# Kernel optimization log

Hardware: AMD Instinct MI355X
Metric: run time of the kernel (lower is better)

Reference implementation:

```python
import jax, jax.numpy as jnp
import numpy as np

DEC_H = 1024
ENC_H_TOTAL = 1024  # enc_hid_size * enc_num_dirs


def setup_inputs() -> dict:
    key = jax.random.key(0)
    ks = jax.random.split(key, 10)
    N, L = 64, 1024
    s = 0.02
    return {
        "dec_h_curr": jax.random.normal(ks[0], (N, DEC_H), jnp.float32),
        "enc_hids": jax.random.normal(ks[1], (N, L, ENC_H_TOTAL), jnp.float32),
        # project_dec_hids: Linear(dec_H, dec_H)
        "W_dec": jax.random.normal(ks[2], (DEC_H, DEC_H), jnp.float32) * s,
        "b_dec": jnp.zeros((DEC_H,), jnp.float32),
        # project_enc_hids: Linear(enc_H*nDir, dec_H)
        "W_enc": jax.random.normal(ks[3], (ENC_H_TOTAL, DEC_H), jnp.float32) * s,
        "b_enc": jnp.zeros((DEC_H,), jnp.float32),
        # project_to_one_dim: Linear(dec_H, 1)
        "W_one": jax.random.normal(ks[4], (DEC_H, 1), jnp.float32) * s,
        "b_one": jnp.zeros((1,), jnp.float32),
        # project_att_hids: Linear(enc_H*nDir, dec_H)
        "W_att": jax.random.normal(ks[5], (ENC_H_TOTAL, DEC_H), jnp.float32) * s,
        "b_att": jnp.zeros((DEC_H,), jnp.float32),
    }


def reference(dec_h_curr, enc_hids, W_dec, b_dec, W_enc, b_enc, W_one, b_one, W_att, b_att):
    # additive (Bahdanau) attention branch
    d = dec_h_curr @ W_dec + b_dec                     # N x dec_H
    e = jnp.einsum('nle,ed->nld', enc_hids, W_enc) + b_enc  # N x L x dec_H
    scores = jnp.einsum('nld,do->nl', jnp.tanh(d[:, None, :] + e), W_one) + b_one[0]  # N x L
    alpha = jax.nn.softmax(scores, axis=-1)            # N x L
    ctx = jnp.einsum('nl,nle->ne', alpha, enc_hids)    # N x enc_H_total
    h_att_curr = ctx @ W_att + b_att                   # N x dec_H
    return h_att_curr, alpha
```

## Files before the change

### kernel.cpp

```cpp
#include <hip/hip_runtime.h>
#include <cstdio>
#include <cstdint>


typedef __bf16 bf16x8 __attribute__((ext_vector_type(8)));
typedef float f32x4 __attribute__((ext_vector_type(4)));
typedef unsigned short us8 __attribute__((ext_vector_type(8)));

static __device__ __forceinline__ unsigned short f2b(float f) {
  union { float f; unsigned u; } v; v.f = f;
  unsigned r = (v.u + 0x7fffu + ((v.u >> 16) & 1u)) >> 16;
  return (unsigned short)r;
}
static __device__ __forceinline__ float b2f(unsigned short u) {
  union { unsigned u; float f; } v; v.u = ((unsigned)u) << 16;
  return v.f;
}
static __device__ __forceinline__ void gl_lds16(const void* g, void* l) {
  __builtin_amdgcn_global_load_lds(
      (const __attribute__((address_space(1))) unsigned int*)g,
      (__attribute__((address_space(3))) unsigned int*)l, 16, 0, 0);
}
static __device__ __forceinline__ float fast_tanh(float x) {
  float ax = __builtin_fminf(__builtin_fabsf(x), 18.0f);
  float u = __builtin_amdgcn_exp2f(ax * 2.88539008177792681f);
  float t = (u - 1.0f) * __builtin_amdgcn_rcpf(u + 1.0f);
  return __builtin_copysignf(t, x);
}

__global__ __launch_bounds__(256) void prep_k(
    const float* __restrict__ enc, unsigned short* __restrict__ Ap,
    const float* __restrict__ W_enc, unsigned short* __restrict__ Bp,
    const float* __restrict__ dec_h, const float* __restrict__ W_dec,
    const float* __restrict__ b_dec, const float* __restrict__ b_enc,
    float* __restrict__ addterm) {
  __shared__ __align__(16) unsigned short tile[8192];
  const int bid = blockIdx.x;
  const int t = threadIdx.x;

  if (bid < 128) {
    const int Tn = bid >> 4, kt = bid & 15;
    #pragma unroll
    for (int it = 0; it < 8; ++it) {
      int idx = it * 256 + t;
      int kk = idx >> 5, n4 = idx & 31;
      const float4 v = *(const float4*)(W_enc + (size_t)(kt * 64 + kk) * 1024 + Tn * 128 + n4 * 4);
      int c = kk >> 3, j = kk & 7;
      #pragma unroll
      for (int x = 0; x < 4; ++x) {
        int mm = n4 * 4 + x;
        float fv = (x == 0) ? v.x : (x == 1) ? v.y : (x == 2) ? v.z : v.w;
        tile[(mm * 8 + (c ^ (mm & 7))) * 8 + j] = f2b(fv);
      }
    }
    __syncthreads();
    #pragma unroll
    for (int it = 0; it < 4; ++it) {
      int p = it * 256 + t;
      int c = p >> 7, m = p & 127;
      us8 v = *(const us8*)&tile[(m * 8 + (c ^ (m & 7))) * 8];
      *(us8*)(Bp + ((size_t)bid * 1024 + p) * 8) = v;
    }
  } else if (bid < 384) {
    const int bid2 = bid - 128;
    const int jb = bid2 & 3, n = bid2 >> 2;
    float* xs = (float*)tile;
    for (int i = t; i < 1024; i += 256) xs[i] = dec_h[n * 1024 + i];
    __syncthreads();
    int j = jb * 256 + t;
    float s = 0.f;
    #pragma unroll 8
    for (int k = 0; k < 1024; ++k) s += xs[k] * W_dec[(size_t)k * 1024 + j];
    addterm[n * 1024 + j] = s + b_dec[j] + b_enc[j];
  } else {
    const int ba = bid - 384;
    const int T = ba >> 4, kt = ba & 15;
    #pragma unroll
    for (int it = 0; it < 8; ++it) {
      int idx = it * 256 + t;
      int m = idx >> 4, c4 = idx & 15;
      const float4 v = *(const float4*)(enc + (size_t)(T * 128 + m) * 1024 + kt * 64 + c4 * 4);
      ushort4 o;
      o.x = f2b(v.x); o.y = f2b(v.y); o.z = f2b(v.z); o.w = f2b(v.w);
      int c = c4 >> 1, half = c4 & 1;
      *(ushort4*)&tile[(m * 8 + (c ^ (m & 7))) * 8 + half * 4] = o;
    }
    __syncthreads();
    #pragma unroll
    for (int it = 0; it < 4; ++it) {
      int p = it * 256 + t;
      int c = p >> 7, m = p & 127;
      us8 v = *(const us8*)&tile[(m * 8 + (c ^ (m & 7))) * 8];
      *(us8*)(Ap + ((size_t)ba * 1024 + p) * 8) = v;
    }
  }
}

__global__ __launch_bounds__(256) void score_gemm(
    const unsigned short* __restrict__ Ap, const unsigned short* __restrict__ Bp,
    const float* __restrict__ addterm, const float* __restrict__ Wone,
    float* __restrict__ spart) {
  __shared__ __align__(16) unsigned short lA[8192];
  __shared__ __align__(16) unsigned short lB[8192];
  const int tid = threadIdx.x;
  const int lane = tid & 63, wave = tid >> 6;
  const int wm = wave >> 1, wn = wave & 1;
  const int q = lane >> 4, r = lane & 15;
  const int flat = blockIdx.x;
  const int nb = (flat >> 3) & 7;
  const int mb = ((flat >> 6) << 3) + (flat & 7);
  const size_t tileM = (size_t)mb * 128;
  const int tileN = nb * 128;

  f32x4 acc[4][4];
  #pragma unroll
  for (int i = 0; i < 4; ++i)
    #pragma unroll
    for (int j = 0; j < 4; ++j) acc[i][j] = (f32x4){0.f, 0.f, 0.f, 0.f};

  const unsigned short* gA[2][2];
  const unsigned short* gB[2][2];
  unsigned short* dA[2][2];
  unsigned short* dB[2][2];
  #pragma unroll
  for (int cc = 0; cc < 2; ++cc) {
    int c = wave * 2 + cc;
    #pragma unroll
    for (int i = 0; i < 2; ++i) {
      gA[cc][i] = Ap + ((((size_t)mb * 16) * 8 + c) * 128 + i * 64 + lane) * 8;
      gB[cc][i] = Bp + ((((size_t)nb * 16) * 8 + c) * 128 + i * 64 + lane) * 8;
      dA[cc][i] = &lA[(c * 128 + i * 64) * 8];
      dB[cc][i] = &lB[(c * 128 + i * 64) * 8];
    }
  }

  for (int kt = 0; kt < 16; ++kt) {
    __syncthreads();
    const size_t ko = (size_t)kt * 8192;
    gl_lds16(gA[0][0] + ko, dA[0][0]);
    gl_lds16(gA[0][1] + ko, dA[0][1]);
    gl_lds16(gA[1][0] + ko, dA[1][0]);
    gl_lds16(gA[1][1] + ko, dA[1][1]);
    gl_lds16(gB[0][0] + ko, dB[0][0]);
    gl_lds16(gB[0][1] + ko, dB[0][1]);
    gl_lds16(gB[1][0] + ko, dB[1][0]);
    gl_lds16(gB[1][1] + ko, dB[1][1]);
    __syncthreads();
    #pragma unroll
    for (int s = 0; s < 2; ++s) {
      bf16x8 af[4], bg[4];
      #pragma unroll
      for (int mi = 0; mi < 4; ++mi)
        af[mi] = *(const bf16x8*)&lA[((s * 4 + q) * 128 + wm * 64 + mi * 16 + r) * 8];
      #pragma unroll
      for (int ni = 0; ni < 4; ++ni)
        bg[ni] = *(const bf16x8*)&lB[((s * 4 + q) * 128 + wn * 64 + ni * 16 + r) * 8];
      #pragma unroll
      for (int mi = 0; mi < 4; ++mi)
        #pragma unroll
        for (int ni = 0; ni < 4; ++ni)
          acc[mi][ni] = __builtin_amdgcn_mfma_f32_16x16x32_bf16(af[mi], bg[ni], acc[mi][ni], 0, 0, 0);
    }
  }

  const int nrow = (int)(tileM >> 10);
  float addv[4], wv[4];
  #pragma unroll
  for (int ni = 0; ni < 4; ++ni) {
    int col = tileN + wn * 64 + ni * 16 + r;
    addv[ni] = addterm[nrow * 1024 + col];
    wv[ni] = Wone[col];
  }
  #pragma unroll
  for (int mi = 0; mi < 4; ++mi) {
    #pragma unroll
    for (int rr = 0; rr < 4; ++rr) {
      float s = 0.f;
      #pragma unroll
      for (int ni = 0; ni < 4; ++ni)
        s += fast_tanh(acc[mi][ni][rr] + addv[ni]) * wv[ni];
      s += __shfl_xor(s, 1);
      s += __shfl_xor(s, 2);
      s += __shfl_xor(s, 4);
      s += __shfl_xor(s, 8);
      if (r == 0) {
        size_t row = tileM + wm * 64 + mi * 16 + q * 4 + rr;
        spart[row * 16 + nb * 2 + wn] = s;
      }
    }
  }
}

__global__ __launch_bounds__(256) void ctx_fused(
    const float* __restrict__ spart, float* __restrict__ alpha,
    const unsigned short* __restrict__ Ap, float* __restrict__ ctx) {
  const int kt = blockIdx.x, n = blockIdx.y, t = threadIdx.x;
  __shared__ float red[8];
  __shared__ float al[1024];

  float sv[4];
  #pragma unroll
  for (int i = 0; i < 4; ++i) {
    int l = i * 256 + t;
    const float4* p = (const float4*)(spart + ((size_t)n * 1024 + l) * 16);
    float4 v0 = p[0], v1 = p[1], v2 = p[2], v3 = p[3];
    sv[i] = (v0.x + v0.y + v0.z + v0.w) + (v1.x + v1.y + v1.z + v1.w) +
            (v2.x + v2.y + v2.z + v2.w) + (v3.x + v3.y + v3.z + v3.w);
  }
  float m = fmaxf(fmaxf(sv[0], sv[1]), fmaxf(sv[2], sv[3]));
  for (int o = 32; o > 0; o >>= 1) m = fmaxf(m, __shfl_xor(m, o));
  if ((t & 63) == 0) red[t >> 6] = m;
  __syncthreads();
  float gm = fmaxf(fmaxf(red[0], red[1]), fmaxf(red[2], red[3]));
  float e[4], s = 0.f;
  #pragma unroll
  for (int i = 0; i < 4; ++i) { e[i] = expf(sv[i] - gm); s += e[i]; }
  for (int o = 32; o > 0; o >>= 1) s += __shfl_xor(s, o);
  if ((t & 63) == 0) red[4 + (t >> 6)] = s;
  __syncthreads();
  float inv = 1.0f / (red[4] + red[5] + red[6] + red[7]);
  #pragma unroll
  for (int i = 0; i < 4; ++i) {
    float a = e[i] * inv;
    al[i * 256 + t] = a;
    if (kt == 0) alpha[(size_t)n * 1024 + i * 256 + t] = a;
  }
  __syncthreads();

  const int c = t >> 5, ls = t & 31;
  float acc[8] = {0.f, 0.f, 0.f, 0.f, 0.f, 0.f, 0.f, 0.f};
  #pragma unroll 4
  for (int lb = 0; lb < 32; ++lb) {
    int l = lb * 32 + ls;
    int M = n * 1024 + l;
    int T = M >> 7, mm = M & 127;
    us8 v = *(const us8*)(Ap + ((((size_t)T * 16 + kt) * 8 + c) * 128 + mm) * 8);
    float w = al[l];
    #pragma unroll
    for (int j = 0; j < 8; ++j) acc[j] += w * b2f(v[j]);
  }
  #pragma unroll
  for (int off = 1; off <= 16; off <<= 1)
    #pragma unroll
    for (int j = 0; j < 8; ++j) acc[j] += __shfl_xor(acc[j], off);
  if (ls == 0) {
    #pragma unroll
    for (int j = 0; j < 8; ++j) ctx[(size_t)n * 1024 + kt * 64 + c * 8 + j] = acc[j];
  }
}

__global__ void hatt_k(const float* __restrict__ ctx, const float* __restrict__ W_att,
                       const float* __restrict__ b_att, float* __restrict__ out) {
  __shared__ float cs[1024];
  int n = blockIdx.y;
  int j = blockIdx.x * 256 + threadIdx.x;
  for (int i = threadIdx.x; i < 1024; i += 256) cs[i] = ctx[(size_t)n * 1024 + i];
  __syncthreads();
  float s = 0.f;
  #pragma unroll 8
  for (int k = 0; k < 1024; ++k) s += cs[k] * W_att[(size_t)k * 1024 + j];
  out[n * 1024 + j] = s + b_att[j];
}

extern "C" void kernel_launch(void* const* d_in, const int* in_sizes, int n_in,
                              void* d_out, int out_size, void* d_ws, size_t ws_size,
                              hipStream_t stream) {
  const float* dec_h = (const float*)d_in[0];
  const float* enc   = (const float*)d_in[1];
  const float* W_dec = (const float*)d_in[2];
  const float* b_dec = (const float*)d_in[3];
  const float* W_enc = (const float*)d_in[4];
  const float* b_enc = (const float*)d_in[5];
  const float* W_one = (const float*)d_in[6];
  const float* W_att = (const float*)d_in[8];
  const float* b_att = (const float*)d_in[9];
  float* out = (float*)d_out;

  char* ws = (char*)d_ws;
  const size_t OFF_A   = 0;
  const size_t OFF_B   = 134217728;
  const size_t OFF_ADD = OFF_B + 2097152;
  const size_t OFF_SP  = OFF_ADD + 262144;
  const size_t OFF_CTX = OFF_SP + 4194304;
  const size_t NEED    = OFF_CTX + 262144;
  if (ws_size < NEED) {
    fprintf(stderr, "kernel_launch: ws too small (%zu < %zu)\n", ws_size, NEED);
    return;
  }
  unsigned short* Ap = (unsigned short*)(ws + OFF_A);
  unsigned short* Bp = (unsigned short*)(ws + OFF_B);
  float* addterm = (float*)(ws + OFF_ADD);
  float* spart   = (float*)(ws + OFF_SP);
  float* ctx     = (float*)(ws + OFF_CTX);
  float* alpha   = out + 65536;

  prep_k<<<8576, 256, 0, stream>>>(enc, Ap, W_enc, Bp, dec_h, W_dec, b_dec, b_enc, addterm);
  score_gemm<<<4096, 256, 0, stream>>>(Ap, Bp, addterm, W_one, spart);
  ctx_fused<<<dim3(16, 64), 256, 0, stream>>>(spart, alpha, Ap, ctx);
  hatt_k<<<dim3(4, 64), 256, 0, stream>>>(ctx, W_att, b_att, out);
}
```

Baseline: 692.7 us.

## Restructure score GEMM into 256x256 double-buffered pipelined tiles; split-K hatt

The score GEMM moves from 128x128 tiles with 4 waves to 256x256 tiles with 8 waves. It adds LDS double buffering, interleaved async global-to-LDS loads placed between MFMA groups, explicit vmcnt waits and s_setprio around MFMA bursts, plus a remapped block order. The intent is to hide load latency and raise arithmetic intensity on the dominant GEMM, at the cost of larger LDS use and hand-tuned waitcnt correctness risk. The hatt kernel is also split along K across 4 waves with a shared-memory reduction, giving 4x more blocks for parallelism.

```diff
diff --git a/kernel.cpp b/kernel.cpp
--- a/kernel.cpp
+++ b/kernel.cpp
@@ -96,83 +96,123 @@
   }
 }
 
-__global__ __launch_bounds__(256) void score_gemm(
+__global__ __launch_bounds__(512, 2) void score_gemm(
     const unsigned short* __restrict__ Ap, const unsigned short* __restrict__ Bp,
     const float* __restrict__ addterm, const float* __restrict__ Wone,
     float* __restrict__ spart) {
-  __shared__ __align__(16) unsigned short lA[8192];
-  __shared__ __align__(16) unsigned short lB[8192];
+  __shared__ __align__(16) unsigned short lA[32768];
+  __shared__ __align__(16) unsigned short lB[32768];
   const int tid = threadIdx.x;
   const int lane = tid & 63, wave = tid >> 6;
-  const int wm = wave >> 1, wn = wave & 1;
+  const int wm = wave >> 2, wn = wave & 3;
   const int q = lane >> 4, r = lane & 15;
+
   const int flat = blockIdx.x;
-  const int nb = (flat >> 3) & 7;
-  const int mb = ((flat >> 6) << 3) + (flat & 7);
-  const size_t tileM = (size_t)mb * 128;
-  const int tileN = nb * 128;
-
-  f32x4 acc[4][4];
-  #pragma unroll
-  for (int i = 0; i < 4; ++i)
+  const int tl = (flat & 7) * 128 + (flat >> 3);
+  const int nb = tl & 3, mb = tl >> 2;
+
+  f32x4 acc[8][4];
+  #pragma unroll
+  for (int i = 0; i < 8; ++i)
     #pragma unroll
     for (int j = 0; j < 4; ++j) acc[i][j] = (f32x4){0.f, 0.f, 0.f, 0.f};
 
-  const unsigned short* gA[2][2];
-  const unsigned short* gB[2][2];
-  unsigned short* dA[2][2];
-  unsigned short* dB[2][2];
-  #pragma unroll
-  for (int cc = 0; cc < 2; ++cc) {
-    int c = wave * 2 + cc;
-    #pragma unroll
-    for (int i = 0; i < 2; ++i) {
-      gA[cc][i] = Ap + ((((size_t)mb * 16) * 8 + c) * 128 + i * 64 + lane) * 8;
-      gB[cc][i] = Bp + ((((size_t)nb * 16) * 8 + c) * 128 + i * 64 + lane) * 8;
-      dA[cc][i] = &lA[(c * 128 + i * 64) * 8];
-      dB[cc][i] = &lB[(c * 128 + i * 64) * 8];
-    }
-  }
-
-  for (int kt = 0; kt < 16; ++kt) {
-    __syncthreads();
-    const size_t ko = (size_t)kt * 8192;
-    gl_lds16(gA[0][0] + ko, dA[0][0]);
-    gl_lds16(gA[0][1] + ko, dA[0][1]);
-    gl_lds16(gA[1][0] + ko, dA[1][0]);
-    gl_lds16(gA[1][1] + ko, dA[1][1]);
-    gl_lds16(gB[0][0] + ko, dB[0][0]);
-    gl_lds16(gB[0][1] + ko, dB[0][1]);
-    gl_lds16(gB[1][0] + ko, dB[1][0]);
-    gl_lds16(gB[1][1] + ko, dB[1][1]);
-    __syncthreads();
-    #pragma unroll
-    for (int s = 0; s < 2; ++s) {
-      bf16x8 af[4], bg[4];
-      #pragma unroll
-      for (int mi = 0; mi < 4; ++mi)
-        af[mi] = *(const bf16x8*)&lA[((s * 4 + q) * 128 + wm * 64 + mi * 16 + r) * 8];
-      #pragma unroll
-      for (int ni = 0; ni < 4; ++ni)
-        bg[ni] = *(const bf16x8*)&lB[((s * 4 + q) * 128 + wn * 64 + ni * 16 + r) * 8];
-      #pragma unroll
-      for (int mi = 0; mi < 4; ++mi)
-        #pragma unroll
-        for (int ni = 0; ni < 4; ++ni)
-          acc[mi][ni] = __builtin_amdgcn_mfma_f32_16x16x32_bf16(af[mi], bg[ni], acc[mi][ni], 0, 0, 0);
-    }
-  }
-
-  const int nrow = (int)(tileM >> 10);
+  const unsigned short* gA0 = Ap + (((size_t)(2 * mb + 0) * 16) * 1024 + tid) * 8;
+  const unsigned short* gA1 = Ap + (((size_t)(2 * mb + 1) * 16) * 1024 + tid) * 8;
+  const unsigned short* gB0 = Bp + (((size_t)(2 * nb + 0) * 16) * 1024 + tid) * 8;
+  const unsigned short* gB1 = Bp + (((size_t)(2 * nb + 1) * 16) * 1024 + tid) * 8;
+
+  const unsigned short* rdA = &lA[(wm * 1024 + q * 128 + r) * 8];
+  const unsigned short* rdB = &lB[((wn >> 1) * 1024 + q * 128 + (wn & 1) * 64 + r) * 8];
+
+  bf16x8 af[4], bg[4];
+
+#define SA(h, t, s) gl_lds16((h ? gA1 : gA0) + ((size_t)(t) * 1024 + (s) * 512) * 8, \
+                             &lA[((((t) & 1) * 2048 + (h) * 1024 + (s) * 512 + wave * 64) * 8)])
+#define SB(h, t, s) gl_lds16((h ? gB1 : gB0) + ((size_t)(t) * 1024 + (s) * 512) * 8, \
+                             &lB[((((t) & 1) * 2048 + (h) * 1024 + (s) * 512 + wave * 64) * 8)])
+#define RD_BG(b, s) { \
+  bg[0] = *(const bf16x8*)&rdB[((b) * 2048 + (s) * 512 +  0) * 8]; \
+  bg[1] = *(const bf16x8*)&rdB[((b) * 2048 + (s) * 512 + 16) * 8]; \
+  bg[2] = *(const bf16x8*)&rdB[((b) * 2048 + (s) * 512 + 32) * 8]; \
+  bg[3] = *(const bf16x8*)&rdB[((b) * 2048 + (s) * 512 + 48) * 8]; }
+#define RD_AF(b, s, mh) { \
+  af[0] = *(const bf16x8*)&rdA[((b) * 2048 + (s) * 512 + (mh) * 64 +  0) * 8]; \
+  af[1] = *(const bf16x8*)&rdA[((b) * 2048 + (s) * 512 + (mh) * 64 + 16) * 8]; \
+  af[2] = *(const bf16x8*)&rdA[((b) * 2048 + (s) * 512 + (mh) * 64 + 32) * 8]; \
+  af[3] = *(const bf16x8*)&rdA[((b) * 2048 + (s) * 512 + (mh) * 64 + 48) * 8]; }
+#define MMA_CORE(mh) \
+  __builtin_amdgcn_s_barrier(); \
+  asm volatile("s_waitcnt lgkmcnt(0)" ::: "memory"); \
+  __builtin_amdgcn_s_setprio(1); \
+  acc[(mh)*4+0][0] = __builtin_amdgcn_mfma_f32_16x16x32_bf16(af[0], bg[0], acc[(mh)*4+0][0], 0, 0, 0); \
+  acc[(mh)*4+0][1] = __builtin_amdgcn_mfma_f32_16x16x32_bf16(af[0], bg[1], acc[(mh)*4+0][1], 0, 0, 0); \
+  acc[(mh)*4+0][2] = __builtin_amdgcn_mfma_f32_16x16x32_bf16(af[0], bg[2], acc[(mh)*4+0][2], 0, 0, 0); \
+  acc[(mh)*4+0][3] = __builtin_amdgcn_mfma_f32_16x16x32_bf16(af[0], bg[3], acc[(mh)*4+0][3], 0, 0, 0); \
+  acc[(mh)*4+1][0] = __builtin_amdgcn_mfma_f32_16x16x32_bf16(af[1], bg[0], acc[(mh)*4+1][0], 0, 0, 0); \
+  acc[(mh)*4+1][1] = __builtin_amdgcn_mfma_f32_16x16x32_bf16(af[1], bg[1], acc[(mh)*4+1][1], 0, 0, 0); \
+  acc[(mh)*4+1][2] = __builtin_amdgcn_mfma_f32_16x16x32_bf16(af[1], bg[2], acc[(mh)*4+1][2], 0, 0, 0); \
+  acc[(mh)*4+1][3] = __builtin_amdgcn_mfma_f32_16x16x32_bf16(af[1], bg[3], acc[(mh)*4+1][3], 0, 0, 0); \
+  acc[(mh)*4+2][0] = __builtin_amdgcn_mfma_f32_16x16x32_bf16(af[2], bg[0], acc[(mh)*4+2][0], 0, 0, 0); \
+  acc[(mh)*4+2][1] = __builtin_amdgcn_mfma_f32_16x16x32_bf16(af[2], bg[1], acc[(mh)*4+2][1], 0, 0, 0); \
+  acc[(mh)*4+2][2] = __builtin_amdgcn_mfma_f32_16x16x32_bf16(af[2], bg[2], acc[(mh)*4+2][2], 0, 0, 0); \
+  acc[(mh)*4+2][3] = __builtin_amdgcn_mfma_f32_16x16x32_bf16(af[2], bg[3], acc[(mh)*4+2][3], 0, 0, 0); \
+  acc[(mh)*4+3][0] = __builtin_amdgcn_mfma_f32_16x16x32_bf16(af[3], bg[0], acc[(mh)*4+3][0], 0, 0, 0); \
+  acc[(mh)*4+3][1] = __builtin_amdgcn_mfma_f32_16x16x32_bf16(af[3], bg[1], acc[(mh)*4+3][1], 0, 0, 0); \
+  acc[(mh)*4+3][2] = __builtin_amdgcn_mfma_f32_16x16x32_bf16(af[3], bg[2], acc[(mh)*4+3][2], 0, 0, 0); \
+  acc[(mh)*4+3][3] = __builtin_amdgcn_mfma_f32_16x16x32_bf16(af[3], bg[3], acc[(mh)*4+3][3], 0, 0, 0); \
+  __builtin_amdgcn_s_setprio(0);
+#define BAR __builtin_amdgcn_s_barrier()
+#define VM4 asm volatile("s_waitcnt vmcnt(4)" ::: "memory")
+#define VM0 asm volatile("s_waitcnt vmcnt(0)" ::: "memory")
+
+  SA(0, 0, 0); SA(1, 0, 0); SB(0, 0, 0); SB(1, 0, 0);
+  SA(0, 0, 1); SA(1, 0, 1); SB(0, 0, 1); SB(1, 0, 1);
+  SA(0, 1, 0); SA(1, 1, 0); SB(0, 1, 0); SB(1, 1, 0);
+  VM4;
+  BAR;
+
+  #pragma unroll 1
+  for (int it = 0; it < 7; ++it) {
+    const int t1 = 2 * it + 1, t2 = 2 * it + 2, t3 = 2 * it + 3;
+    RD_BG(0, 0); RD_AF(0, 0, 0); SA(0, t1, 1); SA(1, t1, 1); MMA_CORE(0); BAR;
+    RD_AF(0, 0, 1); SB(0, t1, 1); SB(1, t1, 1); MMA_CORE(1); BAR;
+    RD_BG(0, 1); RD_AF(0, 1, 0); SA(0, t2, 0); SA(1, t2, 0); MMA_CORE(0); BAR;
+    RD_AF(0, 1, 1); SB(0, t2, 0); SB(1, t2, 0); MMA_CORE(1); VM4; BAR;
+    RD_BG(1, 0); RD_AF(1, 0, 0); SA(0, t2, 1); SA(1, t2, 1); MMA_CORE(0); BAR;
+    RD_AF(1, 0, 1); SB(0, t2, 1); SB(1, t2, 1); MMA_CORE(1); BAR;
+    RD_BG(1, 1); RD_AF(1, 1, 0); SA(0, t3, 0); SA(1, t3, 0); MMA_CORE(0); BAR;
+    RD_AF(1, 1, 1); SB(0, t3, 0); SB(1, t3, 0); MMA_CORE(1); VM4; BAR;
+  }
+
+  RD_BG(0, 0); RD_AF(0, 0, 0); SA(0, 15, 1); SA(1, 15, 1); MMA_CORE(0); BAR;
+  RD_AF(0, 0, 1); SB(0, 15, 1); SB(1, 15, 1); MMA_CORE(1); BAR;
+  RD_BG(0, 1); RD_AF(0, 1, 0); MMA_CORE(0); BAR;
+  RD_AF(0, 1, 1); MMA_CORE(1); VM0; BAR;
+  RD_BG(1, 0); RD_AF(1, 0, 0); MMA_CORE(0); BAR;
+  RD_AF(1, 0, 1); MMA_CORE(1); BAR;
+  RD_BG(1, 1); RD_AF(1, 1, 0); MMA_CORE(0); BAR;
+  RD_AF(1, 1, 1); MMA_CORE(1);
+
+#undef SA
+#undef SB
+#undef RD_BG
+#undef RD_AF
+#undef MMA_CORE
+#undef BAR
+#undef VM4
+#undef VM0
+
+  const int nrow = mb >> 2;
   float addv[4], wv[4];
   #pragma unroll
   for (int ni = 0; ni < 4; ++ni) {
-    int col = tileN + wn * 64 + ni * 16 + r;
+    int col = nb * 256 + wn * 64 + ni * 16 + r;
     addv[ni] = addterm[nrow * 1024 + col];
     wv[ni] = Wone[col];
   }
   #pragma unroll
-  for (int mi = 0; mi < 4; ++mi) {
+  for (int mi = 0; mi < 8; ++mi) {
     #pragma unroll
     for (int rr = 0; rr < 4; ++rr) {
       float s = 0.f;
@@ -184,8 +224,8 @@
       s += __shfl_xor(s, 4);
       s += __shfl_xor(s, 8);
       if (r == 0) {
-        size_t row = tileM + wm * 64 + mi * 16 + q * 4 + rr;
-        spart[row * 16 + nb * 2 + wn] = s;
+        size_t row = (size_t)mb * 256 + wm * 128 + mi * 16 + q * 4 + rr;
+        spart[row * 16 + nb * 4 + wn] = s;
       }
     }
   }
@@ -249,17 +289,28 @@
   }
 }
 
-__global__ void hatt_k(const float* __restrict__ ctx, const float* __restrict__ W_att,
-                       const float* __restrict__ b_att, float* __restrict__ out) {
+__global__ __launch_bounds__(256) void hatt_k(
+    const float* __restrict__ ctx, const float* __restrict__ W_att,
+    const float* __restrict__ b_att, float* __restrict__ out) {
   __shared__ float cs[1024];
-  int n = blockIdx.y;
-  int j = blockIdx.x * 256 + threadIdx.x;
-  for (int i = threadIdx.x; i < 1024; i += 256) cs[i] = ctx[(size_t)n * 1024 + i];
-  __syncthreads();
+  __shared__ float red[4][64];
+  const int n = blockIdx.y;
+  const int jb = blockIdx.x;
+  const int t = threadIdx.x;
+  for (int i = t; i < 1024; i += 256) cs[i] = ctx[(size_t)n * 1024 + i];
+  __syncthreads();
+  const int j = jb * 64 + (t & 63);
+  const int ks = t >> 6;
   float s = 0.f;
+  const float* Wp = W_att + (size_t)(ks * 256) * 1024 + j;
   #pragma unroll 8
-  for (int k = 0; k < 1024; ++k) s += cs[k] * W_att[(size_t)k * 1024 + j];
-  out[n * 1024 + j] = s + b_att[j];
+  for (int k = 0; k < 256; ++k) s += cs[ks * 256 + k] * Wp[(size_t)k * 1024];
+  red[ks][t & 63] = s;
+  __syncthreads();
+  if (t < 64) {
+    out[(size_t)n * 1024 + jb * 64 + t] =
+        red[0][t] + red[1][t] + red[2][t] + red[3][t] + b_att[jb * 64 + t];
+  }
 }
 
 extern "C" void kernel_launch(void* const* d_in, const int* in_sizes, int n_in,
@@ -295,7 +346,7 @@
   float* alpha   = out + 65536;
 
   prep_k<<<8576, 256, 0, stream>>>(enc, Ap, W_enc, Bp, dec_h, W_dec, b_dec, b_enc, addterm);
-  score_gemm<<<4096, 256, 0, stream>>>(Ap, Bp, addterm, W_one, spart);
+  score_gemm<<<1024, 512, 0, stream>>>(Ap, Bp, addterm, W_one, spart);
   ctx_fused<<<dim3(16, 64), 256, 0, stream>>>(spart, alpha, Ap, ctx);
-  hatt_k<<<dim3(4, 64), 256, 0, stream>>>(ctx, W_att, b_att, out);
-}
+  hatt_k<<<dim3(16, 64), 256, 0, stream>>>(ctx, W_att, b_att, out);
+}
```

After: 642.0 us. -7.3%, faster.
